# Kernel optimization log

Measured on AMD Instinct MI355X. Metric: run time of the kernel, lower is better.

## Reference

```python
import jax, jax.numpy as jnp
import numpy as np

EPS = 1e-5  # batch-norm epsilon


def subm_conv(feat, nbrs, W):
    # feat: [N, Cin], nbrs: [N, K] int indices into feat (rulebook), W: [K, Cin, Cout]
    gathered = feat[nbrs]                      # [N, K, Cin]  irregular gather
    return jnp.einsum('nkc,kcd->nd', gathered, W)


def batch_norm(f, gamma, beta):
    # training-mode BN over active sites (scn.BatchNormalization semantics)
    mean = jnp.mean(f, axis=0)
    var = jnp.var(f, axis=0)
    return (f - mean) * jax.lax.rsqrt(var + EPS) * gamma + beta


def setup_inputs() -> dict:
    key = jax.random.key(0)
    k1, k2, k3, k4 = jax.random.split(key, 4)
    N, K, C = 300000, 9, 64
    scale = 1.0 / np.sqrt(K * C)
    return {
        'x': jax.random.normal(k1, (N, C), dtype=jnp.float32),
        'nbrs': jax.random.randint(k2, (N, K), 0, N, dtype=jnp.int32),
        'W1': jax.random.normal(k3, (K, C, C), dtype=jnp.float32) * scale,
        'gamma1': jnp.ones((C,), jnp.float32),
        'beta1': jnp.zeros((C,), jnp.float32),
        'W2': jax.random.normal(k4, (K, C, C), dtype=jnp.float32) * scale,
        'gamma2': jnp.ones((C,), jnp.float32),
        'beta2': jnp.zeros((C,), jnp.float32),
    }


def reference(x, nbrs, W1, gamma1, beta1, W2, gamma2, beta2):
    residual = x
    out = subm_conv(x, nbrs, W1)                       # conv1 (no bias)
    out = jax.nn.relu(batch_norm(out, gamma1, beta1))  # BatchNormReLU
    out = subm_conv(out, nbrs, W2)                     # conv2 (no bias)
    out = batch_norm(out, gamma2, beta2)               # BatchNormalization
    out = jax.nn.relu(out + residual)                  # AddTable + ReLU
    return out
```

## Files before the change

### kernel.cpp

```cpp
#include <hip/hip_runtime.h>

#define NROWS 300000
#define NBLK ((NROWS + 63) / 64)
#define NPART 128

typedef float f32x4 __attribute__((ext_vector_type(4)));
typedef short s16x8 __attribute__((ext_vector_type(8)));
typedef unsigned short u16x8 __attribute__((ext_vector_type(8)));
typedef unsigned short u16x4 __attribute__((ext_vector_type(4)));

__device__ __forceinline__ float bf2f(unsigned short u) {
    return __uint_as_float(((unsigned)u) << 16);
}
__device__ __forceinline__ unsigned short f2bf(float f) {
    unsigned u = __float_as_uint(f);
    u += 0x7FFFu + ((u >> 16) & 1u);
    return (unsigned short)(u >> 16);
}

__global__ __launch_bounds__(256) void x2bf(const float* __restrict__ x,
                                            unsigned short* __restrict__ xb) {
    const int NQ = NROWS * 8;
    for (int i = blockIdx.x * 256 + threadIdx.x; i < NQ; i += gridDim.x * 256) {
        const f32x4 v0 = *(const f32x4*)(x + (size_t)i * 8);
        const f32x4 v1 = *(const f32x4*)(x + (size_t)i * 8 + 4);
        u16x8 o;
        o[0] = f2bf(v0[0]); o[1] = f2bf(v0[1]); o[2] = f2bf(v0[2]); o[3] = f2bf(v0[3]);
        o[4] = f2bf(v1[0]); o[5] = f2bf(v1[1]); o[6] = f2bf(v1[2]); o[7] = f2bf(v1[3]);
        *(u16x8*)(xb + (size_t)i * 8) = o;
    }
}

__global__ __launch_bounds__(256) void w_prep(const float* __restrict__ W1,
                                              const float* __restrict__ W2,
                                              unsigned short* __restrict__ WT1,
                                              unsigned short* __restrict__ WT2) {
    const int i = blockIdx.x * 256 + threadIdx.x;
    if (i < 9 * 4096) {
        const int k = i >> 12, cc = (i >> 6) & 63, d = i & 63;
        const int o = k * 4096 + d * 64 + cc;
        WT1[o] = f2bf(W1[i]);
        WT2[o] = f2bf(W2[i]);
    }
}

template <int CONV>
__global__ __launch_bounds__(256) void conv_mfma(const unsigned short* __restrict__ xb,
                                                 const int* __restrict__ nbrs,
                                                 const unsigned short* __restrict__ WT,
                                                 const float* __restrict__ sb,
                                                 unsigned short* __restrict__ outb) {
    const int tid = threadIdx.x;
    const int l = tid & 63;
    const int w = tid >> 6;
    const int lr = l & 15;
    const int kg = l >> 4;
    const int c00 = kg * 8;

    const int rowA = blockIdx.x * 64 + w * 16 + lr;
    const int rowAc = rowA < NROWS ? rowA : NROWS - 1;

    float s0r[8], b0r[8], s1r[8], b1r[8];
    if (CONV == 2) {
#pragma unroll
        for (int j = 0; j < 8; ++j) {
            s0r[j] = sb[c00 + j];       b0r[j] = sb[64 + c00 + j];
            s1r[j] = sb[32 + c00 + j];  b1r[j] = sb[96 + c00 + j];
        }
    }

    int nb[9];
#pragma unroll
    for (int k = 0; k < 9; ++k) nb[k] = nbrs[rowAc * 9 + k];

    s16x8 raw0[9], raw1[9];
#pragma unroll
    for (int k = 0; k < 9; ++k) {
        const unsigned short* rp = xb + (size_t)nb[k] * 64 + c00;
        raw0[k] = *(const s16x8*)rp;
        raw1[k] = *(const s16x8*)(rp + 32);
    }

    f32x4 acc[4];
#pragma unroll
    for (int d = 0; d < 4; ++d) {
        acc[d][0] = 0.f; acc[d][1] = 0.f; acc[d][2] = 0.f; acc[d][3] = 0.f;
    }

#pragma unroll
    for (int k = 0; k < 9; ++k) {
        s16x8 a0 = raw0[k], a1 = raw1[k];
        if (CONV == 2) {
#pragma unroll
            for (int j = 0; j < 8; ++j) {
                const float f0 = fmaxf(bf2f((unsigned short)a0[j]) * s0r[j] + b0r[j], 0.f);
                const float f1 = fmaxf(bf2f((unsigned short)a1[j]) * s1r[j] + b1r[j], 0.f);
                a0[j] = (short)f2bf(f0);
                a1[j] = (short)f2bf(f1);
            }
        }
        const unsigned short* wp = WT + k * 4096 + lr * 64 + c00;
#pragma unroll
        for (int dj = 0; dj < 4; ++dj) {
            const s16x8 b0 = *(const s16x8*)(wp + dj * 1024);
            const s16x8 b1 = *(const s16x8*)(wp + dj * 1024 + 32);
            acc[dj] = __builtin_amdgcn_mfma_f32_16x16x32_bf16(a0, b0, acc[dj], 0, 0, 0);
            acc[dj] = __builtin_amdgcn_mfma_f32_16x16x32_bf16(a1, b1, acc[dj], 0, 0, 0);
        }
    }

    const int orow0 = blockIdx.x * 64 + w * 16 + kg * 4;
#pragma unroll
    for (int dj = 0; dj < 4; ++dj) {
#pragma unroll
        for (int r = 0; r < 4; ++r) {
            const int orow = orow0 + r;
            if (orow < NROWS) {
                const unsigned short bv = f2bf(acc[dj][r]);
                if (CONV == 2)
                    __builtin_nontemporal_store(bv, &outb[(size_t)orow * 64 + dj * 16 + lr]);
                else
                    outb[(size_t)orow * 64 + dj * 16 + lr] = bv;
            }
        }
    }
}

__global__ __launch_bounds__(256) void bn_stats(const unsigned short* __restrict__ fb,
                                                float* __restrict__ P) {
    const int t = threadIdx.x;
    const int c4 = (t & 15) * 4;
    const int rg = t >> 4;
    float s0 = 0, s1 = 0, s2 = 0, s3 = 0, q0 = 0, q1 = 0, q2 = 0, q3 = 0;
    for (int r = blockIdx.x * 16 + rg; r < NROWS; r += gridDim.x * 16) {
        const u16x4 v = *(const u16x4*)(fb + (size_t)r * 64 + c4);
        const float f0 = bf2f(v[0]), f1 = bf2f(v[1]), f2 = bf2f(v[2]), f3 = bf2f(v[3]);
        s0 += f0; s1 += f1; s2 += f2; s3 += f3;
        q0 += f0 * f0; q1 += f1 * f1; q2 += f2 * f2; q3 += f3 * f3;
    }
    __shared__ float red[16][64];
    red[rg][c4 + 0] = s0; red[rg][c4 + 1] = s1; red[rg][c4 + 2] = s2; red[rg][c4 + 3] = s3;
    __syncthreads();
    if (t < 64) {
        float a = 0;
#pragma unroll
        for (int i = 0; i < 16; ++i) a += red[i][t];
        P[blockIdx.x * 128 + t] = a;
    }
    __syncthreads();
    red[rg][c4 + 0] = q0; red[rg][c4 + 1] = q1; red[rg][c4 + 2] = q2; red[rg][c4 + 3] = q3;
    __syncthreads();
    if (t < 64) {
        float a = 0;
#pragma unroll
        for (int i = 0; i < 16; ++i) a += red[i][t];
        P[blockIdx.x * 128 + 64 + t] = a;
    }
}

__global__ void bn_finalize(const float* __restrict__ P, const float* __restrict__ gamma,
                            const float* __restrict__ beta, float* __restrict__ sb) {
    __shared__ float tot[128];
    const int t = threadIdx.x;
    float a = 0.f;
    for (int p = 0; p < NPART; ++p) a += P[p * 128 + t];
    tot[t] = a;
    __syncthreads();
    if (t < 64) {
        const float mean = tot[t] * (1.0f / NROWS);
        const float var = tot[64 + t] * (1.0f / NROWS) - mean * mean;
        const float sc = gamma[t] * rsqrtf(var + 1e-5f);
        sb[t] = sc;
        sb[64 + t] = beta[t] - mean * sc;
    }
}

__global__ __launch_bounds__(256) void final_out(const unsigned short* __restrict__ o2,
                                                 const float* __restrict__ x,
                                                 const float* __restrict__ sb,
                                                 float* __restrict__ out) {
    const int NQ = NROWS * 16;
    for (int i = blockIdx.x * 256 + threadIdx.x; i < NQ; i += gridDim.x * 256) {
        const int c4 = (i & 15) * 4;
        const u16x4 v = __builtin_nontemporal_load((const u16x4*)(o2 + (size_t)i * 4));
        const f32x4 xv = __builtin_nontemporal_load((const f32x4*)(x + (size_t)i * 4));
        const f32x4 s = *(const f32x4*)(sb + c4);
        const f32x4 b = *(const f32x4*)(sb + 64 + c4);
        f32x4 o;
        o[0] = fmaxf(bf2f(v[0]) * s[0] + b[0] + xv[0], 0.f);
        o[1] = fmaxf(bf2f(v[1]) * s[1] + b[1] + xv[1], 0.f);
        o[2] = fmaxf(bf2f(v[2]) * s[2] + b[2] + xv[2], 0.f);
        o[3] = fmaxf(bf2f(v[3]) * s[3] + b[3] + xv[3], 0.f);
        __builtin_nontemporal_store(o, (f32x4*)(out + (size_t)i * 4));
    }
}

extern "C" void kernel_launch(void* const* d_in, const int* in_sizes, int n_in,
                              void* d_out, int out_size, void* d_ws, size_t ws_size,
                              hipStream_t stream) {
    const float* x      = (const float*)d_in[0];
    const int*   nbrs   = (const int*)d_in[1];
    const float* W1     = (const float*)d_in[2];
    const float* gamma1 = (const float*)d_in[3];
    const float* beta1  = (const float*)d_in[4];
    const float* W2     = (const float*)d_in[5];
    const float* gamma2 = (const float*)d_in[6];
    const float* beta2  = (const float*)d_in[7];
    float* out = (float*)d_out;

    char* ws = (char*)d_ws;
    unsigned short* out2b = (unsigned short*)ws;
    unsigned short* WT1   = (unsigned short*)(ws + 38400000);
    unsigned short* WT2   = (unsigned short*)(ws + 38400000 + 73728);
    float* P1  = (float*)(ws + 38400000 + 147456);
    float* P2  = (float*)(ws + 38400000 + 147456 + 65536);
    float* sb1 = (float*)(ws + 38400000 + 147456 + 131072);
    float* sb2 = sb1 + 128;
    unsigned short* out1b = (unsigned short*)d_out;
    unsigned short* xb    = (unsigned short*)d_out + 19200000;

    x2bf<<<2048, 256, 0, stream>>>(x, xb);
    w_prep<<<144, 256, 0, stream>>>(W1, W2, WT1, WT2);
    conv_mfma<1><<<NBLK, 256, 0, stream>>>(xb, nbrs, WT1, nullptr, out1b);
    bn_stats<<<NPART, 256, 0, stream>>>(out1b, P1);
    bn_finalize<<<1, 128, 0, stream>>>(P1, gamma1, beta1, sb1);
    conv_mfma<2><<<NBLK, 256, 0, stream>>>(out1b, nbrs, WT2, sb1, out2b);
    bn_stats<<<NPART, 256, 0, stream>>>(out2b, P2);
    bn_finalize<<<1, 128, 0, stream>>>(P2, gamma2, beta2, sb2);
    final_out<<<2048, 256, 0, stream>>>(out2b, x, sb2, out);
}
```

Before: 558.4 us.

## Fuse BN statistics into conv epilogues and merge prep kernels

Each conv block now reduces its fp32 accumulators into per-channel sums and sums of squares through wave shuffles and shared memory, and writes per-block partials. This removes the separate bn_stats passes that re-read the bf16 conv outputs. bn_finalize now reduces about 4.7k block partials using 1024 threads, and the x/weight conversion kernels are merged into one launch. The statistics now come from unrounded fp32 values, and the nontemporal hints on the conv2 store and final_out loads are removed.

```diff
diff --git a/kernel.cpp b/kernel.cpp
--- a/kernel.cpp
+++ b/kernel.cpp
@@ -2,7 +2,6 @@
 
 #define NROWS 300000
 #define NBLK ((NROWS + 63) / 64)
-#define NPART 128
 
 typedef float f32x4 __attribute__((ext_vector_type(4)));
 typedef short s16x8 __attribute__((ext_vector_type(8)));
@@ -18,10 +17,21 @@
     return (unsigned short)(u >> 16);
 }
 
-__global__ __launch_bounds__(256) void x2bf(const float* __restrict__ x,
-                                            unsigned short* __restrict__ xb) {
+__global__ __launch_bounds__(256) void prep(const float* __restrict__ x,
+                                            unsigned short* __restrict__ xb,
+                                            const float* __restrict__ W1,
+                                            const float* __restrict__ W2,
+                                            unsigned short* __restrict__ WT1,
+                                            unsigned short* __restrict__ WT2) {
+    const int i0 = blockIdx.x * 256 + threadIdx.x;
+    if (i0 < 9 * 4096) {
+        const int k = i0 >> 12, cc = (i0 >> 6) & 63, d = i0 & 63;
+        const int o = k * 4096 + d * 64 + cc;
+        WT1[o] = f2bf(W1[i0]);
+        WT2[o] = f2bf(W2[i0]);
+    }
     const int NQ = NROWS * 8;
-    for (int i = blockIdx.x * 256 + threadIdx.x; i < NQ; i += gridDim.x * 256) {
+    for (int i = i0; i < NQ; i += gridDim.x * 256) {
         const f32x4 v0 = *(const f32x4*)(x + (size_t)i * 8);
         const f32x4 v1 = *(const f32x4*)(x + (size_t)i * 8 + 4);
         u16x8 o;
@@ -31,25 +41,16 @@
     }
 }
 
-__global__ __launch_bounds__(256) void w_prep(const float* __restrict__ W1,
-                                              const float* __restrict__ W2,
-                                              unsigned short* __restrict__ WT1,
-                                              unsigned short* __restrict__ WT2) {
-    const int i = blockIdx.x * 256 + threadIdx.x;
-    if (i < 9 * 4096) {
-        const int k = i >> 12, cc = (i >> 6) & 63, d = i & 63;
-        const int o = k * 4096 + d * 64 + cc;
-        WT1[o] = f2bf(W1[i]);
-        WT2[o] = f2bf(W2[i]);
-    }
-}
-
 template <int CONV>
 __global__ __launch_bounds__(256) void conv_mfma(const unsigned short* __restrict__ xb,
                                                  const int* __restrict__ nbrs,
                                                  const unsigned short* __restrict__ WT,
                                                  const float* __restrict__ sb,
-                                                 unsigned short* __restrict__ outb) {
+                                                 unsigned short* __restrict__ outb,
+                                                 float* __restrict__ P) {
+    __shared__ float SSum[4][64];
+    __shared__ float SSq[4][64];
+
     const int tid = threadIdx.x;
     const int l = tid & 63;
     const int w = tid >> 6;
@@ -112,63 +113,52 @@
     const int orow0 = blockIdx.x * 64 + w * 16 + kg * 4;
 #pragma unroll
     for (int dj = 0; dj < 4; ++dj) {
+        float sm = 0.f, sq = 0.f;
 #pragma unroll
         for (int r = 0; r < 4; ++r) {
             const int orow = orow0 + r;
             if (orow < NROWS) {
-                const unsigned short bv = f2bf(acc[dj][r]);
-                if (CONV == 2)
-                    __builtin_nontemporal_store(bv, &outb[(size_t)orow * 64 + dj * 16 + lr]);
-                else
-                    outb[(size_t)orow * 64 + dj * 16 + lr] = bv;
+                const float v = acc[dj][r];
+                outb[(size_t)orow * 64 + dj * 16 + lr] = f2bf(v);
+                sm += v; sq += v * v;
             }
         }
-    }
-}
-
-__global__ __launch_bounds__(256) void bn_stats(const unsigned short* __restrict__ fb,
-                                                float* __restrict__ P) {
+        sm += __shfl_xor(sm, 16); sm += __shfl_xor(sm, 32);
+        sq += __shfl_xor(sq, 16); sq += __shfl_xor(sq, 32);
+        if (kg == 0) { SSum[w][dj * 16 + lr] = sm; SSq[w][dj * 16 + lr] = sq; }
+    }
+    __syncthreads();
+    if (tid < 128) {
+        const int c = tid & 63;
+        const float v = (tid < 64)
+            ? SSum[0][c] + SSum[1][c] + SSum[2][c] + SSum[3][c]
+            : SSq[0][c] + SSq[1][c] + SSq[2][c] + SSq[3][c];
+        P[(size_t)blockIdx.x * 128 + tid] = v;
+    }
+}
+
+__global__ __launch_bounds__(1024) void bn_finalize(const float* __restrict__ P,
+                                                    const float* __restrict__ gamma,
+                                                    const float* __restrict__ beta,
+                                                    float* __restrict__ sb) {
+    __shared__ float red[8][128];
     const int t = threadIdx.x;
-    const int c4 = (t & 15) * 4;
-    const int rg = t >> 4;
-    float s0 = 0, s1 = 0, s2 = 0, s3 = 0, q0 = 0, q1 = 0, q2 = 0, q3 = 0;
-    for (int r = blockIdx.x * 16 + rg; r < NROWS; r += gridDim.x * 16) {
-        const u16x4 v = *(const u16x4*)(fb + (size_t)r * 64 + c4);
-        const float f0 = bf2f(v[0]), f1 = bf2f(v[1]), f2 = bf2f(v[2]), f3 = bf2f(v[3]);
-        s0 += f0; s1 += f1; s2 += f2; s3 += f3;
-        q0 += f0 * f0; q1 += f1 * f1; q2 += f2 * f2; q3 += f3 * f3;
-    }
-    __shared__ float red[16][64];
-    red[rg][c4 + 0] = s0; red[rg][c4 + 1] = s1; red[rg][c4 + 2] = s2; red[rg][c4 + 3] = s3;
+    const int c = t & 127;
+    const int s = t >> 7;
+    float a = 0.f;
+    for (int p = s; p < NBLK; p += 8) a += P[(size_t)p * 128 + c];
+    red[s][c] = a;
+    __syncthreads();
+    if (t < 128) {
+        float tot = 0.f;
+#pragma unroll
+        for (int i = 0; i < 8; ++i) tot += red[i][t];
+        red[0][t] = tot;
+    }
     __syncthreads();
     if (t < 64) {
-        float a = 0;
-#pragma unroll
-        for (int i = 0; i < 16; ++i) a += red[i][t];
-        P[blockIdx.x * 128 + t] = a;
-    }
-    __syncthreads();
-    red[rg][c4 + 0] = q0; red[rg][c4 + 1] = q1; red[rg][c4 + 2] = q2; red[rg][c4 + 3] = q3;
-    __syncthreads();
-    if (t < 64) {
-        float a = 0;
-#pragma unroll
-        for (int i = 0; i < 16; ++i) a += red[i][t];
-        P[blockIdx.x * 128 + 64 + t] = a;
-    }
-}
-
-__global__ void bn_finalize(const float* __restrict__ P, const float* __restrict__ gamma,
-                            const float* __restrict__ beta, float* __restrict__ sb) {
-    __shared__ float tot[128];
-    const int t = threadIdx.x;
-    float a = 0.f;
-    for (int p = 0; p < NPART; ++p) a += P[p * 128 + t];
-    tot[t] = a;
-    __syncthreads();
-    if (t < 64) {
-        const float mean = tot[t] * (1.0f / NROWS);
-        const float var = tot[64 + t] * (1.0f / NROWS) - mean * mean;
+        const float mean = red[0][t] * (1.0f / NROWS);
+        const float var = red[0][64 + t] * (1.0f / NROWS) - mean * mean;
         const float sc = gamma[t] * rsqrtf(var + 1e-5f);
         sb[t] = sc;
         sb[64 + t] = beta[t] - mean * sc;
@@ -182,8 +172,8 @@
     const int NQ = NROWS * 16;
     for (int i = blockIdx.x * 256 + threadIdx.x; i < NQ; i += gridDim.x * 256) {
         const int c4 = (i & 15) * 4;
-        const u16x4 v = __builtin_nontemporal_load((const u16x4*)(o2 + (size_t)i * 4));
-        const f32x4 xv = __builtin_nontemporal_load((const f32x4*)(x + (size_t)i * 4));
+        const u16x4 v = *(const u16x4*)(o2 + (size_t)i * 4);
+        const f32x4 xv = *(const f32x4*)(x + (size_t)i * 4);
         const f32x4 s = *(const f32x4*)(sb + c4);
         const f32x4 b = *(const f32x4*)(sb + 64 + c4);
         f32x4 o;
@@ -213,19 +203,16 @@
     unsigned short* WT1   = (unsigned short*)(ws + 38400000);
     unsigned short* WT2   = (unsigned short*)(ws + 38400000 + 73728);
     float* P1  = (float*)(ws + 38400000 + 147456);
-    float* P2  = (float*)(ws + 38400000 + 147456 + 65536);
-    float* sb1 = (float*)(ws + 38400000 + 147456 + 131072);
+    float* P2  = P1 + (size_t)NBLK * 128;
+    float* sb1 = P2 + (size_t)NBLK * 128;
     float* sb2 = sb1 + 128;
     unsigned short* out1b = (unsigned short*)d_out;
     unsigned short* xb    = (unsigned short*)d_out + 19200000;
 
-    x2bf<<<2048, 256, 0, stream>>>(x, xb);
-    w_prep<<<144, 256, 0, stream>>>(W1, W2, WT1, WT2);
-    conv_mfma<1><<<NBLK, 256, 0, stream>>>(xb, nbrs, WT1, nullptr, out1b);
-    bn_stats<<<NPART, 256, 0, stream>>>(out1b, P1);
-    bn_finalize<<<1, 128, 0, stream>>>(P1, gamma1, beta1, sb1);
-    conv_mfma<2><<<NBLK, 256, 0, stream>>>(out1b, nbrs, WT2, sb1, out2b);
-    bn_stats<<<NPART, 256, 0, stream>>>(out2b, P2);
-    bn_finalize<<<1, 128, 0, stream>>>(P2, gamma2, beta2, sb2);
+    prep<<<2048, 256, 0, stream>>>(x, xb, W1, W2, WT1, WT2);
+    conv_mfma<1><<<NBLK, 256, 0, stream>>>(xb, nbrs, WT1, nullptr, out1b, P1);
+    bn_finalize<<<1, 1024, 0, stream>>>(P1, gamma1, beta1, sb1);
+    conv_mfma<2><<<NBLK, 256, 0, stream>>>(out1b, nbrs, WT2, sb1, out2b, P2);
+    bn_finalize<<<1, 1024, 0, stream>>>(P2, gamma2, beta2, sb2);
     final_out<<<2048, 256, 0, stream>>>(out2b, x, sb2, out);
 }
```

After: 754.3 us. +35.1%, slower.
